# Optimization experiments

Hardware: AMD Instinct MI355X
Metric: run time of the kernel (lower is better)

## Reference

```python
import jax, jax.numpy as jnp
import numpy as np

DIM = 1024
CTX_DIM = 1024
HEADS = 8
DIM_HEAD = 64
INNER = HEADS * DIM_HEAD  # 512
EPS = 1e-5


def _layer_norm(x, gamma, beta):
    mu = jnp.mean(x, axis=-1, keepdims=True)
    var = jnp.mean(jnp.square(x - mu), axis=-1, keepdims=True)
    return (x - mu) * jax.lax.rsqrt(var + EPS) * gamma + beta


def setup_inputs() -> dict:
    key = jax.random.key(0)
    ks = jax.random.split(key, 8)
    b, n, m = 4, 2048, 2048
    x = jax.random.normal(ks[0], (b, n, DIM), dtype=jnp.float32)
    context = jax.random.normal(ks[1], (b, m, CTX_DIM), dtype=jnp.float32)
    Wq = jax.random.normal(ks[2], (DIM, INNER), dtype=jnp.float32) / np.sqrt(DIM)
    Wkv = jax.random.normal(ks[3], (CTX_DIM, 2 * INNER), dtype=jnp.float32) / np.sqrt(CTX_DIM)
    Wout = jax.random.normal(ks[4], (INNER, DIM), dtype=jnp.float32) / np.sqrt(INNER)
    bout = jnp.zeros((DIM,), dtype=jnp.float32)
    g1 = jnp.ones((DIM,), dtype=jnp.float32)
    b1 = jnp.zeros((DIM,), dtype=jnp.float32)
    g2 = jnp.ones((CTX_DIM,), dtype=jnp.float32)
    b2 = jnp.zeros((CTX_DIM,), dtype=jnp.float32)
    return {"x": x, "context": context, "g1": g1, "b1": b1, "g2": g2, "b2": b2,
            "Wq": Wq, "Wkv": Wkv, "Wout": Wout, "bout": bout}


def reference(x, context, g1, b1, g2, b2, Wq, Wkv, Wout, bout):
    b, n, _ = x.shape
    m = context.shape[1]
    scale = DIM_HEAD ** -0.5
    xn = _layer_norm(x, g1, b1)
    cn = _layer_norm(context, g2, b2)
    q = xn @ Wq                      # [b, n, inner]
    kv = cn @ Wkv                    # [b, m, 2*inner]
    k, v = jnp.split(kv, 2, axis=-1)
    # split heads: [b, h, seq, d]
    q = q.reshape(b, n, HEADS, DIM_HEAD).transpose(0, 2, 1, 3)
    k = k.reshape(b, m, HEADS, DIM_HEAD).transpose(0, 2, 1, 3)
    v = v.reshape(b, m, HEADS, DIM_HEAD).transpose(0, 2, 1, 3)
    sim = jnp.einsum('bhid,bhjd->bhij', q, k) * scale
    attn = jax.nn.softmax(sim, axis=-1)
    out = jnp.einsum('bhij,bhjd->bhid', attn, v)
    out = out.transpose(0, 2, 1, 3).reshape(b, n, INNER)
    return out @ Wout + bout
```

## Files before the change

kernel.cpp:

```cpp
#include <hip/hip_runtime.h>
#include <hip/hip_bf16.h>

typedef __bf16 bf16_t;
typedef bf16_t bf16x4 __attribute__((ext_vector_type(4)));
typedef bf16_t bf16x8 __attribute__((ext_vector_type(8)));
typedef float floatx4 __attribute__((ext_vector_type(4)));

typedef __attribute__((address_space(1))) const unsigned char* gptr_t;
typedef __attribute__((address_space(3))) unsigned char* lptr_t;

#define BATCH 4
#define SEQ_N 2048
#define SEQ_M 2048
#define DIM 1024
#define INNER 512
#define HEADS 8
#define DHEAD 64
#define QSCALE 0.18033688011112042f

#if __has_builtin(__builtin_amdgcn_exp2f)
#define fast_exp2(x) __builtin_amdgcn_exp2f(x)
#else
#define fast_exp2(x) exp2f(x)
#endif

__device__ __forceinline__ void wtrans_tile(const float* W, bf16_t* Wt,
                                            int K, int N, int n0, int k0, float scale) {
    __shared__ bf16_t T[64][72];
    const int tid = threadIdx.x;
#pragma unroll
    for (int p = 0; p < 2; p++) {
        int r = (tid >> 3) + p * 32;
        int c = (tid & 7) * 8;
        const float* src = W + (size_t)(k0 + r) * N + n0 + c;
        float4 v0 = *(const float4*)src;
        float4 v1 = *(const float4*)(src + 4);
        T[r][c + 0] = (bf16_t)(v0.x * scale); T[r][c + 1] = (bf16_t)(v0.y * scale);
        T[r][c + 2] = (bf16_t)(v0.z * scale); T[r][c + 3] = (bf16_t)(v0.w * scale);
        T[r][c + 4] = (bf16_t)(v1.x * scale); T[r][c + 5] = (bf16_t)(v1.y * scale);
        T[r][c + 6] = (bf16_t)(v1.z * scale); T[r][c + 7] = (bf16_t)(v1.w * scale);
    }
    __syncthreads();
#pragma unroll
    for (int p = 0; p < 2; p++) {
        int rn = (tid >> 3) + p * 32;
        int ck = (tid & 7) * 8;
        bf16x8 v;
#pragma unroll
        for (int i = 0; i < 8; i++) v[i] = T[ck + i][rn];
        *(bf16x8*)(Wt + (size_t)(n0 + rn) * K + k0 + ck) = v;
    }
}

__device__ __forceinline__ void ln_row_wave(const float* in, const float* g,
                                            const float* bt, bf16_t* out, int row) {
    const int lane = threadIdx.x & 63;
    const float4* src = (const float4*)(in + (size_t)row * 1024);
    float4 xv[4];
    float s = 0.f, ss = 0.f;
#pragma unroll
    for (int k = 0; k < 4; k++) {
        xv[k] = src[lane + k * 64];
        s  += xv[k].x + xv[k].y + xv[k].z + xv[k].w;
        ss += xv[k].x * xv[k].x + xv[k].y * xv[k].y + xv[k].z * xv[k].z + xv[k].w * xv[k].w;
    }
#pragma unroll
    for (int off = 32; off > 0; off >>= 1) {
        s  += __shfl_down(s, off);
        ss += __shfl_down(ss, off);
    }
    s  = __shfl(s, 0);
    ss = __shfl(ss, 0);
    const float mu = s * (1.f / 1024.f);
    const float var = ss * (1.f / 1024.f) - mu * mu;
    const float rs = rsqrtf(var + 1e-5f);
    const float4* gp = (const float4*)g;
    const float4* bp = (const float4*)bt;
#pragma unroll
    for (int k = 0; k < 4; k++) {
        float4 gv = gp[lane + k * 64], bv = bp[lane + k * 64];
        bf16x4 o;
        o[0] = (bf16_t)((xv[k].x - mu) * rs * gv.x + bv.x);
        o[1] = (bf16_t)((xv[k].y - mu) * rs * gv.y + bv.y);
        o[2] = (bf16_t)((xv[k].z - mu) * rs * gv.z + bv.z);
        o[3] = (bf16_t)((xv[k].w - mu) * rs * gv.w + bv.w);
        *(bf16x4*)(out + (size_t)row * 1024 + (lane + k * 64) * 4) = o;
    }
}

__global__ __launch_bounds__(256) void prep_kernel(const float* __restrict__ x,
                                                   const float* __restrict__ ctx,
                                                   const float* __restrict__ g1,
                                                   const float* __restrict__ b1,
                                                   const float* __restrict__ g2,
                                                   const float* __restrict__ b2,
                                                   const float* __restrict__ Wq,
                                                   const float* __restrict__ Wkv,
                                                   const float* __restrict__ Wout,
                                                   bf16_t* __restrict__ xn,
                                                   bf16_t* __restrict__ cn,
                                                   bf16_t* __restrict__ Wqt,
                                                   bf16_t* __restrict__ Wkvt,
                                                   bf16_t* __restrict__ Woutt) {
    int id = blockIdx.x;
    if (id < 128) {
        wtrans_tile(Wq, Wqt, 1024, 512, (id & 7) * 64, (id >> 3) * 64, QSCALE);
    } else if (id < 384) {
        int t = id - 128;
        wtrans_tile(Wkv, Wkvt, 1024, 1024, (t & 15) * 64, (t >> 4) * 64, 1.0f);
    } else if (id < 512) {
        int t = id - 384;
        wtrans_tile(Wout, Woutt, 512, 1024, (t & 15) * 64, (t >> 4) * 64, 1.0f);
    } else {
        int row = (id - 512) * 4 + (threadIdx.x >> 6);
        if (row < BATCH * SEQ_N) ln_row_wave(x, g1, b1, xn, row);
        else                     ln_row_wave(ctx, g2, b2, cn, row - BATCH * SEQ_N);
    }
}

template <int NT, int MODE, typename OutT>
__device__ __forceinline__ void gemm_body(const bf16_t* __restrict__ A,
                                          const bf16_t* __restrict__ Bt,
                                          OutT* __restrict__ C,
                                          const float* __restrict__ bias,
                                          int ldC, int K, int row0, int col0) {
    __shared__ bf16_t As[128 * 64];
    __shared__ bf16_t Bs[NT * 64];
    const int tid = threadIdx.x;
    const int wave = tid >> 6, lane = tid & 63;
    constexpr int WC = NT / 2;
    constexpr int NJ = WC / 16;
    const int wr = (wave >> 1) * 64, wc = (wave & 1) * WC;
    const int quad = lane >> 4, l16 = lane & 15;

    floatx4 acc[4][NJ] = {};

    for (int k0 = 0; k0 < K; k0 += 64) {
#pragma unroll
        for (int p = 0; p < 4; p++) {
            int cA = p * 256 + wave * 64 + lane;
            int rA = cA >> 3, kc = (cA & 7) * 8;
            __builtin_amdgcn_global_load_lds(
                (gptr_t)(A + (size_t)(row0 + rA) * K + k0 + kc),
                (lptr_t)(As + (size_t)(p * 256 + wave * 64) * 8), 16, 0, 0);
            if (p < NT / 32)
                __builtin_amdgcn_global_load_lds(
                    (gptr_t)(Bt + (size_t)(col0 + rA) * K + k0 + kc),
                    (lptr_t)(Bs + (size_t)(p * 256 + wave * 64) * 8), 16, 0, 0);
        }
        __syncthreads();
#pragma unroll
        for (int kt = 0; kt < 2; kt++) {
            bf16x8 aF[4], bF[NJ];
#pragma unroll
            for (int i = 0; i < 4; i++)
                aF[i] = *(bf16x8*)&As[(wr + i * 16 + l16) * 64 + kt * 32 + quad * 8];
#pragma unroll
            for (int j = 0; j < NJ; j++)
                bF[j] = *(bf16x8*)&Bs[(wc + j * 16 + l16) * 64 + kt * 32 + quad * 8];
#pragma unroll
            for (int i = 0; i < 4; i++)
#pragma unroll
                for (int j = 0; j < NJ; j++) {
                    if (MODE == 0)
                        acc[i][j] = __builtin_amdgcn_mfma_f32_16x16x32_bf16(
                            aF[i], bF[j], acc[i][j], 0, 0, 0);
                    else
                        acc[i][j] = __builtin_amdgcn_mfma_f32_16x16x32_bf16(
                            bF[j], aF[i], acc[i][j], 0, 0, 0);
                }
        }
        __syncthreads();
    }

    if (MODE == 0) {
#pragma unroll
        for (int i = 0; i < 4; i++)
#pragma unroll
            for (int j = 0; j < NJ; j++) {
                int col = col0 + wc + j * 16 + l16;
                float bv = bias ? bias[col] : 0.f;
#pragma unroll
                for (int r = 0; r < 4; r++) {
                    int row = row0 + wr + i * 16 + quad * 4 + r;
                    C[(size_t)row * ldC + col] = (OutT)(acc[i][j][r] + bv);
                }
            }
    } else {
        bf16_t* Tw = (wave < 2 ? As : Bs) + (wave & 1) * 4096;
#pragma unroll
        for (int i = 0; i < 4; i++)
#pragma unroll
            for (int j = 0; j < 4; j++)
#pragma unroll
                for (int r = 0; r < 4; r++)
                    Tw[(j * 16 + quad * 4 + r) * 64 + i * 16 + l16] = (bf16_t)acc[i][j][r];
        __syncthreads();
        const int grow = row0 + wr;
        const int bat = grow >> 11, gm = (grow & 2047) + l16 * 4;
#pragma unroll
        for (int dd = 0; dd < 16; dd++) {
            int d = dd * 4 + quad;
            bf16x4 v = *(bf16x4*)&Tw[d * 64 + l16 * 4];
            int gd = col0 + wc + d - 512;
            *(bf16x4*)(C + ((size_t)bat * 512 + gd) * 2048 + gm) = v;
        }
    }
}

__global__ __launch_bounds__(256) void gemm_qkv_kernel(const bf16_t* __restrict__ xn,
                                                       const bf16_t* __restrict__ cn,
                                                       const bf16_t* __restrict__ Wqt,
                                                       const bf16_t* __restrict__ Wkvt,
                                                       bf16_t* __restrict__ qb,
                                                       bf16_t* __restrict__ kvb,
                                                       bf16_t* __restrict__ Vtg) {
    const int f = blockIdx.x;
    const int lb = (f & 7) * 96 + (f >> 3);
    const int bx = lb % 12;
    const int row0 = (lb / 12) * 128;
    if (bx < 4)
        gemm_body<128, 0, bf16_t>(xn, Wqt, qb, nullptr, 512, DIM, row0, bx * 128);
    else if (bx < 8)
        gemm_body<128, 0, bf16_t>(cn, Wkvt, kvb, nullptr, 512, DIM, row0, (bx - 4) * 128);
    else
        gemm_body<128, 1, bf16_t>(cn, Wkvt, Vtg, nullptr, 0, DIM, row0, (bx - 4) * 128);
}

__global__ __launch_bounds__(256) void gemm_out_kernel(const bf16_t* __restrict__ ao,
                                                       const bf16_t* __restrict__ Woutt,
                                                       float* __restrict__ out,
                                                       const float* __restrict__ bias) {
    const int f = blockIdx.x;
    const int lb = (f & 7) * 128 + (f >> 3);
    gemm_body<64, 0, float>(ao, Woutt, out, bias, DIM, INNER,
                            (lb >> 4) * 128, (lb & 15) * 64);
}

__global__ __launch_bounds__(256) void attn_kernel(const bf16_t* __restrict__ q,
                                                   const bf16_t* __restrict__ kv,
                                                   const bf16_t* __restrict__ Vtg,
                                                   bf16_t* __restrict__ o) {
    __shared__ bf16_t Qs[128 * 64];
    __shared__ bf16_t Ks[2][64 * 64];
    __shared__ bf16_t Vs[2][64 * 64];

    const int f = blockIdx.x;
    const int lb = ((f & 7) << 6) | (f >> 3);
    const int b = lb >> 7, h = (lb >> 4) & 7;
    const int n0 = (lb & 15) * 128;

    const int tid = threadIdx.x;
    const int wave = tid >> 6, lane = tid & 63;
    const int quad = lane >> 4, l16 = lane & 15;
    const int swz = (l16 & 7) << 3;

    const int sr = tid >> 3;
    const int sc = (tid & 7) * 8;
    const int scs = sc ^ ((sr & 7) << 3);

    const int rloc = lane >> 3;
    const int srccol = ((lane & 7) ^ rloc) << 3;
    const bf16_t* kgl = kv + ((size_t)(b * SEQ_M) + wave * 16 + rloc) * 512
                           + h * DHEAD + srccol;
    const bf16_t* vgl = Vtg + ((size_t)((b * HEADS + h) * DHEAD)
                               + wave * 16 + rloc) * SEQ_M + srccol;

#pragma unroll
    for (int p = 0; p < 2; p++) {
        __builtin_amdgcn_global_load_lds(
            (gptr_t)(kgl + (size_t)(p * 8) * 512),
            (lptr_t)(Ks[0] + (wave * 2 + p) * 512), 16, 0, 0);
        __builtin_amdgcn_global_load_lds(
            (gptr_t)(vgl + (size_t)(p * 8) * SEQ_M),
            (lptr_t)(Vs[0] + (wave * 2 + p) * 512), 16, 0, 0);
    }

#pragma unroll
    for (int p = 0; p < 4; p++) {
        int r = sr + p * 32;
        *(bf16x8*)&Qs[r * 64 + scs] =
            *(const bf16x8*)(q + (size_t)(b * SEQ_N + n0 + r) * INNER + h * DHEAD + sc);
    }

    bf16x8 bOnes;
    {
        bf16_t ov = (l16 == 0) ? (bf16_t)1.0f : (bf16_t)0.0f;
#pragma unroll
        for (int i = 0; i < 8; i++) bOnes[i] = ov;
    }

    __syncthreads();

    bf16x8 aQ0[2], aQ1[2];
#pragma unroll
    for (int kt = 0; kt < 2; kt++) {
        aQ0[kt] = *(bf16x8*)&Qs[(wave * 32 + l16) * 64 + ((kt * 32 + quad * 8) ^ swz)];
        aQ1[kt] = *(bf16x8*)&Qs[(wave * 32 + 16 + l16) * 64 + ((kt * 32 + quad * 8) ^ swz)];
    }

    kgl += (size_t)64 * 512;
    vgl += 64;
#pragma unroll
    for (int p = 0; p < 2; p++) {
        __builtin_amdgcn_global_load_lds(
            (gptr_t)(kgl + (size_t)(p * 8) * 512),
            (lptr_t)(Ks[1] + (wave * 2 + p) * 512), 16, 0, 0);
        __builtin_amdgcn_global_load_lds(
            (gptr_t)(vgl + (size_t)(p * 8) * SEQ_M),
            (lptr_t)(Vs[1] + (wave * 2 + p) * 512), 16, 0, 0);
    }

    bf16_t* Pw0 = Qs + wave * 2048;
    bf16_t* Pw1 = Pw0 + 1024;

    floatx4 oacc0[5] = {}, oacc1[5] = {};

    int cur = 0;
    for (int it = 0; it < SEQ_M / 64; ++it) {
        floatx4 s0[4] = {}, s1[4] = {};
        __builtin_amdgcn_s_setprio(1);
#pragma unroll
        for (int kt = 0; kt < 2; kt++)
#pragma unroll
            for (int jt = 0; jt < 4; jt++) {
                bf16x8 aK = *(bf16x8*)&Ks[cur][(jt * 16 + l16) * 64 +
                                              ((kt * 32 + quad * 8) ^ swz)];
                s0[jt] = __builtin_amdgcn_mfma_f32_16x16x32_bf16(aK, aQ0[kt], s0[jt], 0, 0, 0);
                s1[jt] = __builtin_amdgcn_mfma_f32_16x16x32_bf16(aK, aQ1[kt], s1[jt], 0, 0, 0);
            }
        __builtin_amdgcn_s_setprio(0);

#pragma unroll
        for (int jt = 0; jt < 4; jt++) {
            bf16x4 pk0, pk1;
#pragma unroll
            for (int r = 0; r < 4; r++) {
                pk0[r] = (bf16_t)fast_exp2(s0[jt][r]);
                pk1[r] = (bf16_t)fast_exp2(s1[jt][r]);
            }
            int pc = (jt * 16 + quad * 4) ^ swz;
            *(bf16x4*)&Pw0[l16 * 64 + pc] = pk0;
            *(bf16x4*)&Pw1[l16 * 64 + pc] = pk1;
        }

        __builtin_amdgcn_s_setprio(1);
#pragma unroll
        for (int kt = 0; kt < 2; kt++) {
            int ac = (kt * 32 + quad * 8) ^ swz;
            bf16x8 aP0 = *(bf16x8*)&Pw0[l16 * 64 + ac];
            bf16x8 aP1 = *(bf16x8*)&Pw1[l16 * 64 + ac];
#pragma unroll
            for (int dt = 0; dt < 4; dt++) {
                bf16x8 bV = *(bf16x8*)&Vs[cur][(dt * 16 + l16) * 64 + ac];
                oacc0[dt] = __builtin_amdgcn_mfma_f32_16x16x32_bf16(aP0, bV, oacc0[dt], 0, 0, 0);
                oacc1[dt] = __builtin_amdgcn_mfma_f32_16x16x32_bf16(aP1, bV, oacc1[dt], 0, 0, 0);
            }
            oacc0[4] = __builtin_amdgcn_mfma_f32_16x16x32_bf16(aP0, bOnes, oacc0[4], 0, 0, 0);
            oacc1[4] = __builtin_amdgcn_mfma_f32_16x16x32_bf16(aP1, bOnes, oacc1[4], 0, 0, 0);
        }
        __builtin_amdgcn_s_setprio(0);

        __syncthreads();

        kgl += (size_t)64 * 512;
        vgl += 64;
#pragma unroll
        for (int p = 0; p < 2; p++) {
            __builtin_amdgcn_global_load_lds(
                (gptr_t)(kgl + (size_t)(p * 8) * 512),
                (lptr_t)(Ks[cur] + (wave * 2 + p) * 512), 16, 0, 0);
            __builtin_amdgcn_global_load_lds(
                (gptr_t)(vgl + (size_t)(p * 8) * SEQ_M),
                (lptr_t)(Vs[cur] + (wave * 2 + p) * 512), 16, 0, 0);
        }
        cur ^= 1;
    }

#pragma unroll
    for (int set = 0; set < 2; set++) {
        const floatx4* oa = set == 0 ? oacc0 : oacc1;
        float inv[4];
#pragma unroll
        for (int r = 0; r < 4; r++) {
            float l = __shfl(oa[4][r], (int)(lane & 48));
            inv[r] = 1.0f / l;
        }
#pragma unroll
        for (int dt = 0; dt < 4; dt++)
#pragma unroll
            for (int r = 0; r < 4; r++) {
                int row = n0 + wave * 32 + set * 16 + quad * 4 + r;
                int col = h * DHEAD + dt * 16 + l16;
                o[(size_t)(b * SEQ_N + row) * INNER + col] =
                    (bf16_t)(oa[dt][r] * inv[r]);
            }
    }
}

extern "C" void kernel_launch(void* const* d_in, const int* in_sizes, int n_in,
                              void* d_out, int out_size, void* d_ws, size_t ws_size,
                              hipStream_t stream) {
    const float* x    = (const float*)d_in[0];
    const float* ctx  = (const float*)d_in[1];
    const float* g1   = (const float*)d_in[2];
    const float* b1   = (const float*)d_in[3];
    const float* g2   = (const float*)d_in[4];
    const float* b2   = (const float*)d_in[5];
    const float* Wq   = (const float*)d_in[6];
    const float* Wkv  = (const float*)d_in[7];
    const float* Wout = (const float*)d_in[8];
    const float* bout = (const float*)d_in[9];
    float* out = (float*)d_out;

    const int rows = BATCH * SEQ_N;
    bf16_t* xn    = (bf16_t*)d_ws;
    bf16_t* cn    = xn + (size_t)rows * DIM;
    bf16_t* qb    = cn + (size_t)rows * DIM;
    bf16_t* kvb   = qb + (size_t)rows * INNER;
    bf16_t* Vtg   = kvb + (size_t)rows * INNER;
    bf16_t* Wqt   = Vtg + (size_t)rows * INNER;
    bf16_t* Wkvt  = Wqt + (size_t)INNER * DIM;
    bf16_t* Woutt = Wkvt + (size_t)(2 * INNER) * DIM;
    bf16_t* o_attn = xn;

    prep_kernel<<<512 + (2 * rows) / 4, 256, 0, stream>>>(
        x, ctx, g1, b1, g2, b2, Wq, Wkv, Wout, xn, cn, Wqt, Wkvt, Woutt);
    gemm_qkv_kernel<<<768, 256, 0, stream>>>(
        xn, cn, Wqt, Wkvt, qb, kvb, Vtg);
    attn_kernel<<<512, 256, 0, stream>>>(qb, kvb, Vtg, o_attn);
    gemm_out_kernel<<<1024, 256, 0, stream>>>(o_attn, Woutt, out, bout);
}
```

Before: 239.4 us.

## Software-pipeline QK^T one tile ahead with triple-buffered K/V in attention

The attention loop now computes the QK^T scores for the next K tile in the same MFMA-priority region as the current tile's PV product. This lets the score MFMAs overlap the exp/P-store work instead of serialising them. K/V staging moves from double to triple buffering so the next tile is resident one iteration earlier, and a prefetch lambda advances the global pointers. Launch bounds now request 2 blocks per CU. The extra score accumulators raise register pressure and could cause spills, and LDS use grows to 64KB per block.

```diff
diff --git a/kernel.cpp b/kernel.cpp
--- a/kernel.cpp
+++ b/kernel.cpp
@@ -237,13 +237,13 @@
                             (lb >> 4) * 128, (lb & 15) * 64);
 }
 
-__global__ __launch_bounds__(256) void attn_kernel(const bf16_t* __restrict__ q,
-                                                   const bf16_t* __restrict__ kv,
-                                                   const bf16_t* __restrict__ Vtg,
-                                                   bf16_t* __restrict__ o) {
+__global__ __launch_bounds__(256, 2) void attn_kernel(const bf16_t* __restrict__ q,
+                                                      const bf16_t* __restrict__ kv,
+                                                      const bf16_t* __restrict__ Vtg,
+                                                      bf16_t* __restrict__ o) {
     __shared__ bf16_t Qs[128 * 64];
-    __shared__ bf16_t Ks[2][64 * 64];
-    __shared__ bf16_t Vs[2][64 * 64];
+    __shared__ bf16_t Ks[3][64 * 64];
+    __shared__ bf16_t Vs[3][64 * 64];
 
     const int f = blockIdx.x;
     const int lb = ((f & 7) << 6) | (f >> 3);
@@ -266,15 +266,22 @@
     const bf16_t* vgl = Vtg + ((size_t)((b * HEADS + h) * DHEAD)
                                + wave * 16 + rloc) * SEQ_M + srccol;
 
-#pragma unroll
-    for (int p = 0; p < 2; p++) {
-        __builtin_amdgcn_global_load_lds(
-            (gptr_t)(kgl + (size_t)(p * 8) * 512),
-            (lptr_t)(Ks[0] + (wave * 2 + p) * 512), 16, 0, 0);
-        __builtin_amdgcn_global_load_lds(
-            (gptr_t)(vgl + (size_t)(p * 8) * SEQ_M),
-            (lptr_t)(Vs[0] + (wave * 2 + p) * 512), 16, 0, 0);
-    }
+    auto STAGE = [&](bf16_t* KD, bf16_t* VD) {
+#pragma unroll
+        for (int p = 0; p < 2; p++) {
+            __builtin_amdgcn_global_load_lds(
+                (gptr_t)(kgl + (size_t)(p * 8) * 512),
+                (lptr_t)(KD + (wave * 2 + p) * 512), 16, 0, 0);
+            __builtin_amdgcn_global_load_lds(
+                (gptr_t)(vgl + (size_t)(p * 8) * SEQ_M),
+                (lptr_t)(VD + (wave * 2 + p) * 512), 16, 0, 0);
+        }
+        kgl += (size_t)64 * 512;
+        vgl += 64;
+    };
+
+    STAGE(Ks[0], Vs[0]);
+    STAGE(Ks[1], Vs[1]);
 
 #pragma unroll
     for (int p = 0; p < 4; p++) {
@@ -299,38 +306,33 @@
         aQ1[kt] = *(bf16x8*)&Qs[(wave * 32 + 16 + l16) * 64 + ((kt * 32 + quad * 8) ^ swz)];
     }
 
-    kgl += (size_t)64 * 512;
-    vgl += 64;
-#pragma unroll
-    for (int p = 0; p < 2; p++) {
-        __builtin_amdgcn_global_load_lds(
-            (gptr_t)(kgl + (size_t)(p * 8) * 512),
-            (lptr_t)(Ks[1] + (wave * 2 + p) * 512), 16, 0, 0);
-        __builtin_amdgcn_global_load_lds(
-            (gptr_t)(vgl + (size_t)(p * 8) * SEQ_M),
-            (lptr_t)(Vs[1] + (wave * 2 + p) * 512), 16, 0, 0);
-    }
+    STAGE(Ks[2], Vs[2]);
+
+    auto QK = [&](const bf16_t* KB, floatx4* d0, floatx4* d1) {
+#pragma unroll
+        for (int kt = 0; kt < 2; kt++)
+#pragma unroll
+            for (int jt = 0; jt < 4; jt++) {
+                bf16x8 aK = *(bf16x8*)&KB[(jt * 16 + l16) * 64 +
+                                          ((kt * 32 + quad * 8) ^ swz)];
+                d0[jt] = __builtin_amdgcn_mfma_f32_16x16x32_bf16(aK, aQ0[kt], d0[jt], 0, 0, 0);
+                d1[jt] = __builtin_amdgcn_mfma_f32_16x16x32_bf16(aK, aQ1[kt], d1[jt], 0, 0, 0);
+            }
+    };
 
     bf16_t* Pw0 = Qs + wave * 2048;
     bf16_t* Pw1 = Pw0 + 1024;
 
     floatx4 oacc0[5] = {}, oacc1[5] = {};
 
-    int cur = 0;
+    bf16_t *cK = Ks[0], *cV = Vs[0];
+    bf16_t *nK = Ks[1], *nV = Vs[1];
+    bf16_t *xK = Ks[2], *xV = Vs[2];
+
+    floatx4 s0[4] = {}, s1[4] = {};
+    QK(cK, s0, s1);
+
     for (int it = 0; it < SEQ_M / 64; ++it) {
-        floatx4 s0[4] = {}, s1[4] = {};
-        __builtin_amdgcn_s_setprio(1);
-#pragma unroll
-        for (int kt = 0; kt < 2; kt++)
-#pragma unroll
-            for (int jt = 0; jt < 4; jt++) {
-                bf16x8 aK = *(bf16x8*)&Ks[cur][(jt * 16 + l16) * 64 +
-                                              ((kt * 32 + quad * 8) ^ swz)];
-                s0[jt] = __builtin_amdgcn_mfma_f32_16x16x32_bf16(aK, aQ0[kt], s0[jt], 0, 0, 0);
-                s1[jt] = __builtin_amdgcn_mfma_f32_16x16x32_bf16(aK, aQ1[kt], s1[jt], 0, 0, 0);
-            }
-        __builtin_amdgcn_s_setprio(0);
-
 #pragma unroll
         for (int jt = 0; jt < 4; jt++) {
             bf16x4 pk0, pk1;
@@ -345,6 +347,9 @@
         }
 
         __builtin_amdgcn_s_setprio(1);
+        floatx4 t0[4] = {}, t1[4] = {};
+        QK(nK, t0, t1);
+
 #pragma unroll
         for (int kt = 0; kt < 2; kt++) {
             int ac = (kt * 32 + quad * 8) ^ swz;
@@ -352,7 +357,7 @@
             bf16x8 aP1 = *(bf16x8*)&Pw1[l16 * 64 + ac];
 #pragma unroll
             for (int dt = 0; dt < 4; dt++) {
-                bf16x8 bV = *(bf16x8*)&Vs[cur][(dt * 16 + l16) * 64 + ac];
+                bf16x8 bV = *(bf16x8*)&cV[(dt * 16 + l16) * 64 + ac];
                 oacc0[dt] = __builtin_amdgcn_mfma_f32_16x16x32_bf16(aP0, bV, oacc0[dt], 0, 0, 0);
                 oacc1[dt] = __builtin_amdgcn_mfma_f32_16x16x32_bf16(aP1, bV, oacc1[dt], 0, 0, 0);
             }
@@ -363,18 +368,13 @@
 
         __syncthreads();
 
-        kgl += (size_t)64 * 512;
-        vgl += 64;
-#pragma unroll
-        for (int p = 0; p < 2; p++) {
-            __builtin_amdgcn_global_load_lds(
-                (gptr_t)(kgl + (size_t)(p * 8) * 512),
-                (lptr_t)(Ks[cur] + (wave * 2 + p) * 512), 16, 0, 0);
-            __builtin_amdgcn_global_load_lds(
-                (gptr_t)(vgl + (size_t)(p * 8) * SEQ_M),
-                (lptr_t)(Vs[cur] + (wave * 2 + p) * 512), 16, 0, 0);
-        }
-        cur ^= 1;
+        STAGE(cK, cV);
+
+        bf16_t* t;
+        t = cK; cK = nK; nK = xK; xK = t;
+        t = cV; cV = nV; nV = xV; xV = t;
+#pragma unroll
+        for (int jt = 0; jt < 4; jt++) { s0[jt] = t0[jt]; s1[jt] = t1[jt]; }
     }
 
 #pragma unroll
```

New measurement: 231.7 us. 3.2% less time.
